# Optimization experiments

Measured on AMD Instinct MI355X. Metric: run time of the kernel, lower is better.

The kernel has to match this reference:

```python
import jax, jax.numpy as jnp
import numpy as np

B, S = 2, 2048
HID = 2560
NH, NKV, HD = 20, 5, 128
GROUPS = NH // NKV  # 4
THETA = 500000.0
RMS_EPS = 1e-6  # RMSNorm default eps used for attn_sub_norm
NEG_INF = -1e9


def pack_ternary(key, M, K):
    """Pack ternary weights {-1,0,1} (stored as trits {0,1,2}) into SIMD
    block-interleaved uint8 layout: per 128-elem block, byte j holds
    weights j+0 (bits 6:7), j+32 (4:5), j+64 (2:3), j+96 (0:1)."""
    t = jax.random.randint(key, (M, K), 0, 3).astype(jnp.uint8)
    t = t.reshape(M, K // 128, 4, 32)
    byte = (t[:, :, 0] << 6) | (t[:, :, 1] << 4) | (t[:, :, 2] << 2) | t[:, :, 3]
    return byte.reshape(M, K // 4)


def unpack_ternary(packed):
    """Inverse of pack_ternary -> float weights in {-1,0,1}. (M, K//4) -> (M, K)."""
    M, Kp = packed.shape
    nb = Kp // 32
    b = packed.reshape(M, nb, 32)
    fields = jnp.stack([(b >> 6) & 3, (b >> 4) & 3, (b >> 2) & 3, b & 3], axis=2)
    return fields.reshape(M, nb * 128).astype(jnp.float32) - 1.0


def bitlinear(x, packed, scale):
    w = unpack_ternary(packed) * scale  # (out, in)
    return jnp.einsum('bsi,oi->bso', x, w)


def rotate_half(x):
    h = x.shape[-1] // 2
    return jnp.concatenate([-x[..., h:], x[..., :h]], axis=-1)


def rms_norm(x, w, eps=RMS_EPS):
    var = jnp.mean(jnp.square(x.astype(jnp.float32)), axis=-1, keepdims=True)
    return (w * (x * jax.lax.rsqrt(var + eps))).astype(x.dtype)


def setup_inputs() -> dict:
    key = jax.random.key(0)
    ks = jax.random.split(key, 6)
    hidden_states = jax.random.normal(ks[0], (B, S, HID), dtype=jnp.float32)
    causal = jnp.tril(jnp.ones((S, S), dtype=bool))
    attention_mask = jnp.where(causal, 0.0, NEG_INF).astype(jnp.float32)[None, None]
    return {
        'hidden_states': hidden_states,
        'attention_mask': attention_mask,
        'q_w': pack_ternary(ks[1], NH * HD, HID),
        'k_w': pack_ternary(ks[2], NKV * HD, HID),
        'v_w': pack_ternary(ks[3], NKV * HD, HID),
        'o_w': pack_ternary(ks[4], HID, NH * HD),
        'q_scale': jnp.float32(0.02),
        'k_scale': jnp.float32(0.02),
        'v_scale': jnp.float32(0.02),
        'o_scale': jnp.float32(0.02),
        'attn_norm_w': jnp.ones((NH * HD,), dtype=jnp.float32),
    }


def reference(hidden_states, attention_mask, q_w, k_w, v_w, o_w,
              q_scale, k_scale, v_scale, o_scale, attn_norm_w):
    bsz, seq_len, _ = hidden_states.shape
    q = bitlinear(hidden_states, q_w, q_scale)
    k = bitlinear(hidden_states, k_w, k_scale)
    v = bitlinear(hidden_states, v_w, v_scale)
    q = q.reshape(bsz, seq_len, NH, HD).transpose(0, 2, 1, 3)    # (b,h,s,d)
    k = k.reshape(bsz, seq_len, NKV, HD).transpose(0, 2, 1, 3)
    v = v.reshape(bsz, seq_len, NKV, HD).transpose(0, 2, 1, 3)
    # rotary embedding
    inv_freq = 1.0 / (THETA ** (jnp.arange(0, HD, 2, dtype=jnp.float32) / HD))
    t = jnp.arange(seq_len, dtype=jnp.float32)
    freqs = t[:, None] * inv_freq[None, :]            # (s, d/2)
    emb = jnp.concatenate([freqs, freqs], axis=-1)    # (s, d)
    cos, sin = jnp.cos(emb), jnp.sin(emb)
    q = q * cos + rotate_half(q) * sin
    k = k * cos + rotate_half(k) * sin
    # GQA: repeat kv heads
    k = jnp.repeat(k, GROUPS, axis=1)
    v = jnp.repeat(v, GROUPS, axis=1)
    scores = jnp.einsum('bhqd,bhkd->bhqk', q, k) / np.sqrt(HD).astype(np.float32)
    scores = scores + attention_mask
    attn = jax.nn.softmax(scores.astype(jnp.float32), axis=-1).astype(q.dtype)
    out = jnp.einsum('bhqk,bhkd->bhqd', attn, v)
    out = out.transpose(0, 2, 1, 3).reshape(bsz, seq_len, NH * HD)
    out = rms_norm(out, attn_norm_w)
    return bitlinear(out, o_w, o_scale)
```

## Files before the change

kernel.cpp:

```cpp
#include <hip/hip_runtime.h>
#include <cstdint>
#include <cstddef>

typedef __bf16 bf16x8 __attribute__((ext_vector_type(8)));
typedef float  f32x4  __attribute__((ext_vector_type(4)));
typedef int    i32x4  __attribute__((ext_vector_type(4)));
typedef unsigned short u16x4 __attribute__((ext_vector_type(4)));

#define DEV __device__ __forceinline__
#define NEGINF (-__builtin_inff())

DEV uint16_t f2bf(float f) {
  union { float f; uint32_t u; } v; v.f = f;
  uint32_t u = v.u;
  u += 0x7FFFu + ((u >> 16) & 1u);
  return (uint16_t)(u >> 16);
}
DEV float bf2f(uint16_t h) {
  union { uint32_t u; float f; } v; v.u = ((uint32_t)h) << 16;
  return v.f;
}

DEV void gload_lds16(const void* g, void* l) {
  __builtin_amdgcn_global_load_lds(
      (const __attribute__((address_space(1))) void*)g,
      (__attribute__((address_space(3))) void*)l, 16, 0, 0);
}


__global__ void k_f32_to_bf16(const float* __restrict__ in, uint16_t* __restrict__ out, int n4) {
  int i = blockIdx.x * blockDim.x + threadIdx.x;
  if (i >= n4) return;
  f32x4 v = *(const f32x4*)(in + (size_t)i * 4);
  u16x4 o;
  o[0] = f2bf(v[0]); o[1] = f2bf(v[1]); o[2] = f2bf(v[2]); o[3] = f2bf(v[3]);
  *(u16x4*)(out + (size_t)i * 4) = o;
}

__global__ void k_unpack(const uint32_t* __restrict__ p, uint16_t* __restrict__ w, int total, int Kq) {
  int idx = blockIdx.x * blockDim.x + threadIdx.x;
  if (idx >= total) return;
  int row = idx / Kq, pc = idx - row * Kq;
  int blk = pc >> 5, j = pc & 31;
  uint32_t b = p[idx] & 0xFFu;
  size_t base = (size_t)row * (size_t)(Kq * 4) + (size_t)blk * 128 + j;
  w[base]      = f2bf((float)((b >> 6) & 3u) - 1.0f);
  w[base + 32] = f2bf((float)((b >> 4) & 3u) - 1.0f);
  w[base + 64] = f2bf((float)((b >> 2) & 3u) - 1.0f);
  w[base + 96] = f2bf((float)(b & 3u) - 1.0f);
}

__global__ void k_rope_table(float* __restrict__ cosT, float* __restrict__ sinT) {
  int idx = blockIdx.x * blockDim.x + threadIdx.x;
  int s = idx >> 6, i = idx & 63;
  float inv = expf((float)i * (-13.122363377404328f / 64.0f));
  float fr = (float)s * inv;
  cosT[idx] = cosf(fr);
  sinT[idx] = sinf(fr);
}

__global__ void k_rope(uint16_t* __restrict__ buf, const float* __restrict__ cosT,
                       const float* __restrict__ sinT, int H, int total) {
  int idx = blockIdx.x * blockDim.x + threadIdx.x;
  if (idx >= total) return;
  int d = idx & 63;
  int t = idx >> 6;
  int h = t % H;
  int row = t / H;
  int s = row & 2047;
  size_t base = (size_t)row * (size_t)(H * 128) + (size_t)h * 128 + d;
  float x1 = bf2f(buf[base]), x2 = bf2f(buf[base + 64]);
  float c = cosT[(s << 6) + d], sn = sinT[(s << 6) + d];
  buf[base]      = f2bf(x1 * c - x2 * sn);
  buf[base + 64] = f2bf(x2 * c + x1 * sn);
}

template<int MODE>
__global__ __launch_bounds__(256, 2)
void k_gemm(const uint16_t* __restrict__ A, const uint16_t* __restrict__ W,
            uint16_t* __restrict__ Qo, uint16_t* __restrict__ Ko, uint16_t* __restrict__ Vo,
            float* __restrict__ Fo,
            const float* __restrict__ s0p, const float* __restrict__ s1p, const float* __restrict__ s2p,
            int M, int N, int K)
{
  __shared__ uint16_t As[128 * 64];
  __shared__ uint16_t Bs[128 * 64];
  const int tid = threadIdx.x;
  const int n0 = blockIdx.x * 128, m0 = blockIdx.y * 128;
  const int lane = tid & 63, w = tid >> 6;
  const int wm = (w >> 1) * 64, wn = (w & 1) * 64;
  const int lr = lane & 15, lg = lane >> 4, lk = lg * 8;
  const size_t K2 = (size_t)K * 2;
  f32x4 acc[4][4] = {};

  const int srow = tid >> 3;
  const int cprime = ((tid & 7) * 16) ^ ((srow & 7) << 4);
  const uint8_t* Ag = (const uint8_t*)A + (size_t)(m0 + srow) * K2 + cprime;
  const uint8_t* Wg = (const uint8_t*)W + (size_t)(n0 + srow) * K2 + cprime;
  char* Al = (char*)As + w * 1024;
  char* Bl = (char*)Bs + w * 1024;

  for (size_t k0b = 0; k0b < K2; k0b += 128) {
    #pragma unroll
    for (int i = 0; i < 4; ++i)
      gload_lds16(Ag + (size_t)(i * 32) * K2 + k0b, Al + i * 4096);
    #pragma unroll
    for (int i = 0; i < 4; ++i)
      gload_lds16(Wg + (size_t)(i * 32) * K2 + k0b, Bl + i * 4096);
    __syncthreads();
    #pragma unroll
    for (int kc = 0; kc < 64; kc += 32) {
      bf16x8 a[4], b[4];
      #pragma unroll
      for (int i = 0; i < 4; ++i) {
        const int r = wm + i * 16 + lr;
        a[i] = *(const bf16x8*)((const char*)As + r * 128 + (((kc + lk) * 2) ^ ((r & 7) << 4)));
      }
      #pragma unroll
      for (int j = 0; j < 4; ++j) {
        const int r = wn + j * 16 + lr;
        b[j] = *(const bf16x8*)((const char*)Bs + r * 128 + (((kc + lk) * 2) ^ ((r & 7) << 4)));
      }
      #pragma unroll
      for (int i = 0; i < 4; ++i)
        #pragma unroll
        for (int j = 0; j < 4; ++j)
          acc[i][j] = __builtin_amdgcn_mfma_f32_16x16x32_bf16(a[i], b[j], acc[i][j], 0, 0, 0);
    }
    __syncthreads();
  }

  if (MODE == 0) {
    const float qs = *s0p, ks = *s1p, vs = *s2p;
    #pragma unroll
    for (int i = 0; i < 4; ++i) {
      const int rowb = m0 + wm + i * 16 + lg * 4;
      #pragma unroll
      for (int j = 0; j < 4; ++j) {
        const int col = n0 + wn + j * 16 + lr;
        #pragma unroll
        for (int r = 0; r < 4; ++r) {
          const int rr = rowb + r;
          const float v = acc[i][j][r];
          if (col < 2560) {
            Qo[(size_t)rr * 2560 + col] = f2bf(v * qs);
          } else if (col < 3200) {
            Ko[(size_t)rr * 640 + (col - 2560)] = f2bf(v * ks);
          } else {
            const int n2 = col - 3200;
            const int kvh = n2 >> 7, d = n2 & 127;
            const int bb = rr >> 11, ss = rr & 2047;
            Vo[(((size_t)(bb * 5 + kvh) * 128 + d) << 11) + ss] = f2bf(v * vs);
          }
        }
      }
    }
  } else {
    const float os = *s0p;
    #pragma unroll
    for (int i = 0; i < 4; ++i) {
      const int rowb = m0 + wm + i * 16 + lg * 4;
      #pragma unroll
      for (int j = 0; j < 4; ++j) {
        const int col = n0 + wn + j * 16 + lr;
        #pragma unroll
        for (int r = 0; r < 4; ++r)
          Fo[(size_t)(rowb + r) * N + col] = acc[i][j][r] * os;
      }
    }
  }
}

__global__ __launch_bounds__(256)
void k_attn(const uint16_t* __restrict__ Q, const uint16_t* __restrict__ Kb,
            const uint16_t* __restrict__ Vt, uint16_t* __restrict__ Ob)
{
  __shared__ char Klds[2][16384];
  __shared__ char Vlds[2][16384];
  __shared__ uint16_t p_lds[4][16][88];

  const int lin = blockIdx.x + (blockIdx.y << 6);
  const int gslot = (lin & 7) * 80 + (lin >> 3);
  const int p = gslot & 63;
  const int bk = gslot >> 6;
  const int b = bk / 5, kvh = bk - b * 5;

  const int tid = threadIdx.x, lane = tid & 63, w = tid >> 6;
  const int lr = lane & 15, lg = lane >> 4, lk = lg * 8;
  const int h = kvh * 4 + w;
  uint16_t (*pl)[88] = p_lds[w];
  const int kswz = (lr & 7) << 4;

  const uint8_t* Kg = (const uint8_t*)(Kb + (size_t)b * 2048 * 640 + (size_t)kvh * 128);
  const uint8_t* Vg = (const uint8_t*)(Vt + ((size_t)(b * 5 + kvh) * 128) * 2048);

  const int krow = tid >> 4;
  const int kcol = ((tid & 15) * 16) ^ ((krow & 7) << 4);
  const int vrow = tid >> 3;
  const int vcol = ((tid & 7) * 16) ^ ((vrow & 7) << 4);
  const int dst16 = tid * 16;

  const float C = 0.127531019577f;

  #pragma unroll 1
  for (int sel = 0; sel < 2; ++sel) {
    const int st = sel ? (127 - p) : p;
    const int q0 = st * 16;
    const int ns = (q0 + 79) >> 6;

    bf16x8 qf[4];
    {
      const size_t qbase = ((size_t)(b * 2048 + q0 + lr)) * 2560 + (size_t)h * 128 + lk;
      #pragma unroll
      for (int c = 0; c < 4; ++c) qf[c] = *(const bf16x8*)&Q[qbase + c * 32];
    }
    asm volatile("s_waitcnt vmcnt(0)" ::: "memory");

    {
      const uint8_t* Ks = Kg + (size_t)krow * 1280 + kcol;
      const uint8_t* Vs = Vg + (size_t)vrow * 4096 + vcol;
      char* Kd = Klds[0] + dst16;
      char* Vd = Vlds[0] + dst16;
      #pragma unroll
      for (int i = 0; i < 4; ++i) gload_lds16(Ks + (size_t)i * 16 * 1280, Kd + i * 4096);
      #pragma unroll
      for (int i = 0; i < 4; ++i) gload_lds16(Vs + (size_t)i * 32 * 4096, Vd + i * 4096);
    }

    int cur = 0;
    float m = NEGINF, l = 0.f;
    f32x4 oa[8] = {};

    #pragma unroll 1
    for (int stp = 0; stp < ns; ++stp) {
      const int k0 = stp * 64;
      if (stp + 1 < ns) {
        const int kn = k0 + 64;
        const uint8_t* Ks = Kg + (size_t)(kn + krow) * 1280 + kcol;
        const uint8_t* Vs = Vg + (size_t)vrow * 4096 + (size_t)kn * 2 + vcol;
        char* Kd = Klds[cur ^ 1] + dst16;
        char* Vd = Vlds[cur ^ 1] + dst16;
        #pragma unroll
        for (int i = 0; i < 4; ++i) gload_lds16(Ks + (size_t)i * 16 * 1280, Kd + i * 4096);
        #pragma unroll
        for (int i = 0; i < 4; ++i) gload_lds16(Vs + (size_t)i * 32 * 4096, Vd + i * 4096);
        asm volatile("s_waitcnt vmcnt(8)" ::: "memory");
      } else {
        asm volatile("s_waitcnt vmcnt(0)" ::: "memory");
      }
      __syncthreads();

      const char* Kc = Klds[cur];
      const char* Vc = Vlds[cur];
      const bool bound = (k0 + 64 >= q0 + 16);

      f32x4 sa[4] = {};
      #pragma unroll
      for (int t = 0; t < 4; ++t) {
        #pragma unroll
        for (int c = 0; c < 4; ++c) {
          bf16x8 kf = *(const bf16x8*)(Kc + (t * 16 + lr) * 256 + ((c * 64 + lg * 16) ^ kswz));
          sa[t] = __builtin_amdgcn_mfma_f32_16x16x32_bf16(kf, qf[c], sa[t], 0, 0, 0);
        }
      }
      float u[16];
      if (bound) {
        #pragma unroll
        for (int t = 0; t < 4; ++t)
          #pragma unroll
          for (int r = 0; r < 4; ++r)
            u[t * 4 + r] = (k0 + t * 16 + lg * 4 + r <= q0 + lr) ? sa[t][r] * C : NEGINF;
      } else {
        #pragma unroll
        for (int t = 0; t < 4; ++t)
          #pragma unroll
          for (int r = 0; r < 4; ++r)
            u[t * 4 + r] = sa[t][r] * C;
      }
      float m01 = fmaxf(u[0], u[1]),   m23 = fmaxf(u[2], u[3]);
      float m45 = fmaxf(u[4], u[5]),   m67 = fmaxf(u[6], u[7]);
      float m89 = fmaxf(u[8], u[9]),   mab = fmaxf(u[10], u[11]);
      float mcd = fmaxf(u[12], u[13]), mef = fmaxf(u[14], u[15]);
      float mx = fmaxf(fmaxf(fmaxf(m01, m23), fmaxf(m45, m67)),
                       fmaxf(fmaxf(m89, mab), fmaxf(mcd, mef)));
      mx = fmaxf(mx, __shfl_xor(mx, 16));
      mx = fmaxf(mx, __shfl_xor(mx, 32));
      const float mn = fmaxf(m, mx);
      const float resc = __builtin_exp2f(m - mn);
      m = mn;
      float pv[16];
      #pragma unroll
      for (int i = 0; i < 16; ++i) pv[i] = __builtin_exp2f(u[i] - mn);
      float s0 = (pv[0] + pv[1]) + (pv[2] + pv[3]);
      float s1 = (pv[4] + pv[5]) + (pv[6] + pv[7]);
      float s2 = (pv[8] + pv[9]) + (pv[10] + pv[11]);
      float s3 = (pv[12] + pv[13]) + (pv[14] + pv[15]);
      l = l * resc + ((s0 + s1) + (s2 + s3));
      #pragma unroll
      for (int t = 0; t < 4; ++t) {
        union { __bf16 b4[4]; unsigned long long u64; } pk;
        #pragma unroll
        for (int r = 0; r < 4; ++r) pk.b4[r] = (__bf16)pv[t * 4 + r];
        *(unsigned long long*)&pl[lr][t * 16 + lg * 4] = pk.u64;
      }
      #pragma unroll
      for (int dc = 0; dc < 8; ++dc) {
        oa[dc][0] *= resc; oa[dc][1] *= resc; oa[dc][2] *= resc; oa[dc][3] *= resc;
      }
      bf16x8 pa0 = *(const bf16x8*)&pl[lr][lk];
      bf16x8 pa1 = *(const bf16x8*)&pl[lr][32 + lk];
      #pragma unroll
      for (int dc = 0; dc < 8; ++dc) {
        bf16x8 vf0 = *(const bf16x8*)(Vc + (dc * 16 + lr) * 128 + ((lg * 16) ^ kswz));
        bf16x8 vf1 = *(const bf16x8*)(Vc + (dc * 16 + lr) * 128 + ((64 + lg * 16) ^ kswz));
        oa[dc] = __builtin_amdgcn_mfma_f32_16x16x32_bf16(vf0, pa0, oa[dc], 0, 0, 0);
        oa[dc] = __builtin_amdgcn_mfma_f32_16x16x32_bf16(vf1, pa1, oa[dc], 0, 0, 0);
      }
      __syncthreads();
      cur ^= 1;
    }

    float lf = l;
    lf += __shfl_xor(lf, 16);
    lf += __shfl_xor(lf, 32);
    const float inv = 1.0f / lf;
    const size_t obase = ((size_t)(b * 2048 + q0 + lr)) * 2560 + (size_t)h * 128;
    #pragma unroll
    for (int dc = 0; dc < 8; ++dc) {
      union { __bf16 b4[4]; unsigned long long u64; } ok;
      #pragma unroll
      for (int r = 0; r < 4; ++r) ok.b4[r] = (__bf16)(oa[dc][r] * inv);
      *(unsigned long long*)&Ob[obase + dc * 16 + lg * 4] = ok.u64;
    }
  }
}

__global__ __launch_bounds__(256)
void k_rmsnorm(const uint16_t* __restrict__ X, const float* __restrict__ g, uint16_t* __restrict__ Y)
{
  const int row = blockIdx.x;
  const int tid = threadIdx.x;
  const uint16_t* x = X + (size_t)row * 2560;
  float ss = 0.f;
  #pragma unroll
  for (int it = 0; it < 10; ++it) {
    const int i = tid + it * 256;
    const float v = bf2f(x[i]);
    ss += v * v;
  }
  #pragma unroll
  for (int off = 1; off < 64; off <<= 1) ss += __shfl_xor(ss, off, 64);
  __shared__ float sred[4];
  if ((tid & 63) == 0) sred[tid >> 6] = ss;
  __syncthreads();
  const float tot = sred[0] + sred[1] + sred[2] + sred[3];
  const float rs = rsqrtf(tot * (1.0f / 2560.0f) + 1e-6f);
  uint16_t* y = Y + (size_t)row * 2560;
  #pragma unroll
  for (int it = 0; it < 10; ++it) {
    const int i = tid + it * 256;
    y[i] = f2bf(bf2f(x[i]) * rs * g[i]);
  }
}

extern "C" void kernel_launch(void* const* d_in, const int* in_sizes, int n_in,
                              void* d_out, int out_size, void* d_ws, size_t ws_size,
                              hipStream_t stream)
{
  const float*    x     = (const float*)d_in[0];
  const uint32_t* qw    = (const uint32_t*)d_in[2];
  const uint32_t* kw    = (const uint32_t*)d_in[3];
  const uint32_t* vw    = (const uint32_t*)d_in[4];
  const uint32_t* ow    = (const uint32_t*)d_in[5];
  const float*    qs    = (const float*)d_in[6];
  const float*    ks    = (const float*)d_in[7];
  const float*    vs    = (const float*)d_in[8];
  const float*    os    = (const float*)d_in[9];
  const float*    gnorm = (const float*)d_in[10];

  char* ws = (char*)d_ws;
  uint16_t* xb   = (uint16_t*)(ws + 0);
  uint16_t* wqkv = (uint16_t*)(ws + 20971520);
  uint16_t* owb  = (uint16_t*)(ws + 40632320);
  float*    cosT = (float*)   (ws + 53739520);
  float*    sinT = (float*)   (ws + 54263808);
  uint16_t* Qb   = (uint16_t*)(ws + 54788096);
  uint16_t* Kb   = (uint16_t*)(ws + 75759616);
  uint16_t* Vt   = (uint16_t*)(ws + 81002496);

  k_f32_to_bf16<<<10240, 256, 0, stream>>>(x, xb, 2621440);
  k_unpack<<<6400, 256, 0, stream>>>(qw, wqkv, 1638400, 640);
  k_unpack<<<1600, 256, 0, stream>>>(kw, wqkv + (size_t)2560 * 2560, 409600, 640);
  k_unpack<<<1600, 256, 0, stream>>>(vw, wqkv + (size_t)3200 * 2560, 409600, 640);
  k_unpack<<<6400, 256, 0, stream>>>(ow, owb, 1638400, 640);
  k_rope_table<<<512, 256, 0, stream>>>(cosT, sinT);

  k_gemm<0><<<dim3(30, 32), 256, 0, stream>>>(xb, wqkv, Qb, Kb, Vt, nullptr,
                                              qs, ks, vs, 4096, 3840, 2560);
  k_rope<<<20480, 256, 0, stream>>>(Qb, cosT, sinT, 20, 5242880);
  k_rope<<<5120, 256, 0, stream>>>(Kb, cosT, sinT, 5, 1310720);

  k_attn<<<dim3(64, 10), 256, 0, stream>>>(Qb, Kb, Vt, xb);

  k_rmsnorm<<<4096, 256, 0, stream>>>(xb, gnorm, Qb);

  k_gemm<1><<<dim3(20, 32), 256, 0, stream>>>(Qb, owb, nullptr, nullptr, nullptr,
                                              (float*)d_out, os, nullptr, nullptr,
                                              4096, 2560, 2560);
}
```

Measured before the change: 335.3 us.

## Double-buffer GEMM LDS tiles and load attention V directly to registers

The GEMM now double-buffers its A/W LDS tiles, prefetching the next K-slab while computing on the current one, with a single barrier per iteration instead of two. In attention, V is no longer staged through LDS. Each wave loads its V fragments straight from global memory into registers, and only K is double-buffered in LDS. The next K prefetch is issued mid-iteration, and s_setprio is raised around the MFMA blocks. This aims to hide global latency and cut LDS traffic and barriers. The cost is more registers and uncoalesced, duplicated V global reads across the four waves.

```diff
diff --git a/kernel.cpp b/kernel.cpp
--- a/kernel.cpp
+++ b/kernel.cpp
@@ -83,8 +83,8 @@
             const float* __restrict__ s0p, const float* __restrict__ s1p, const float* __restrict__ s2p,
             int M, int N, int K)
 {
-  __shared__ uint16_t As[128 * 64];
-  __shared__ uint16_t Bs[128 * 64];
+  __shared__ uint16_t As[2][128 * 64];
+  __shared__ uint16_t Bs[2][128 * 64];
   const int tid = threadIdx.x;
   const int n0 = blockIdx.x * 128, m0 = blockIdx.y * 128;
   const int lane = tid & 63, w = tid >> 6;
@@ -97,29 +97,44 @@
   const int cprime = ((tid & 7) * 16) ^ ((srow & 7) << 4);
   const uint8_t* Ag = (const uint8_t*)A + (size_t)(m0 + srow) * K2 + cprime;
   const uint8_t* Wg = (const uint8_t*)W + (size_t)(n0 + srow) * K2 + cprime;
-  char* Al = (char*)As + w * 1024;
-  char* Bl = (char*)Bs + w * 1024;
-
-  for (size_t k0b = 0; k0b < K2; k0b += 128) {
-    #pragma unroll
-    for (int i = 0; i < 4; ++i)
-      gload_lds16(Ag + (size_t)(i * 32) * K2 + k0b, Al + i * 4096);
-    #pragma unroll
-    for (int i = 0; i < 4; ++i)
-      gload_lds16(Wg + (size_t)(i * 32) * K2 + k0b, Bl + i * 4096);
-    __syncthreads();
+  const int woff = w * 1024;
+
+  #pragma unroll
+  for (int i = 0; i < 4; ++i)
+    gload_lds16(Ag + (size_t)(i * 32) * K2, (char*)As[0] + woff + i * 4096);
+  #pragma unroll
+  for (int i = 0; i < 4; ++i)
+    gload_lds16(Wg + (size_t)(i * 32) * K2, (char*)Bs[0] + woff + i * 4096);
+
+  const int NT = K >> 6;
+  int cur = 0;
+  #pragma unroll 1
+  for (int t = 0; t < NT; ++t) {
+    asm volatile("s_waitcnt vmcnt(0)" ::: "memory");
+    __builtin_amdgcn_s_barrier();
+    if (t + 1 < NT) {
+      const size_t kb = (size_t)(t + 1) * 128;
+      #pragma unroll
+      for (int i = 0; i < 4; ++i)
+        gload_lds16(Ag + (size_t)(i * 32) * K2 + kb, (char*)As[cur ^ 1] + woff + i * 4096);
+      #pragma unroll
+      for (int i = 0; i < 4; ++i)
+        gload_lds16(Wg + (size_t)(i * 32) * K2 + kb, (char*)Bs[cur ^ 1] + woff + i * 4096);
+    }
+    const char* Ac = (const char*)As[cur];
+    const char* Bc = (const char*)Bs[cur];
     #pragma unroll
     for (int kc = 0; kc < 64; kc += 32) {
       bf16x8 a[4], b[4];
       #pragma unroll
       for (int i = 0; i < 4; ++i) {
         const int r = wm + i * 16 + lr;
-        a[i] = *(const bf16x8*)((const char*)As + r * 128 + (((kc + lk) * 2) ^ ((r & 7) << 4)));
+        a[i] = *(const bf16x8*)(Ac + r * 128 + (((kc + lk) * 2) ^ ((r & 7) << 4)));
       }
       #pragma unroll
       for (int j = 0; j < 4; ++j) {
         const int r = wn + j * 16 + lr;
-        b[j] = *(const bf16x8*)((const char*)Bs + r * 128 + (((kc + lk) * 2) ^ ((r & 7) << 4)));
+        b[j] = *(const bf16x8*)(Bc + r * 128 + (((kc + lk) * 2) ^ ((r & 7) << 4)));
       }
       #pragma unroll
       for (int i = 0; i < 4; ++i)
@@ -127,7 +142,7 @@
         for (int j = 0; j < 4; ++j)
           acc[i][j] = __builtin_amdgcn_mfma_f32_16x16x32_bf16(a[i], b[j], acc[i][j], 0, 0, 0);
     }
-    __syncthreads();
+    cur ^= 1;
   }
 
   if (MODE == 0) {
@@ -176,7 +191,6 @@
             const uint16_t* __restrict__ Vt, uint16_t* __restrict__ Ob)
 {
   __shared__ char Klds[2][16384];
-  __shared__ char Vlds[2][16384];
   __shared__ uint16_t p_lds[4][16][88];
 
   const int lin = blockIdx.x + (blockIdx.y << 6);
@@ -191,13 +205,11 @@
   uint16_t (*pl)[88] = p_lds[w];
   const int kswz = (lr & 7) << 4;
 
-  const uint8_t* Kg = (const uint8_t*)(Kb + (size_t)b * 2048 * 640 + (size_t)kvh * 128);
-  const uint8_t* Vg = (const uint8_t*)(Vt + ((size_t)(b * 5 + kvh) * 128) * 2048);
+  const uint8_t*  Kg    = (const uint8_t*)(Kb + (size_t)b * 2048 * 640 + (size_t)kvh * 128);
+  const uint16_t* Vbase = Vt + ((size_t)(b * 5 + kvh) * 128) * 2048;
 
   const int krow = tid >> 4;
   const int kcol = ((tid & 15) * 16) ^ ((krow & 7) << 4);
-  const int vrow = tid >> 3;
-  const int vcol = ((tid & 7) * 16) ^ ((vrow & 7) << 4);
   const int dst16 = tid * 16;
 
   const float C = 0.127531019577f;
@@ -208,23 +220,20 @@
     const int q0 = st * 16;
     const int ns = (q0 + 79) >> 6;
 
+    __builtin_amdgcn_s_barrier();
+
     bf16x8 qf[4];
     {
       const size_t qbase = ((size_t)(b * 2048 + q0 + lr)) * 2560 + (size_t)h * 128 + lk;
       #pragma unroll
       for (int c = 0; c < 4; ++c) qf[c] = *(const bf16x8*)&Q[qbase + c * 32];
     }
-    asm volatile("s_waitcnt vmcnt(0)" ::: "memory");
 
     {
       const uint8_t* Ks = Kg + (size_t)krow * 1280 + kcol;
-      const uint8_t* Vs = Vg + (size_t)vrow * 4096 + vcol;
-      char* Kd = Klds[0] + dst16;
-      char* Vd = Vlds[0] + dst16;
-      #pragma unroll
-      for (int i = 0; i < 4; ++i) gload_lds16(Ks + (size_t)i * 16 * 1280, Kd + i * 4096);
-      #pragma unroll
-      for (int i = 0; i < 4; ++i) gload_lds16(Vs + (size_t)i * 32 * 4096, Vd + i * 4096);
+      #pragma unroll
+      for (int i = 0; i < 4; ++i)
+        gload_lds16(Ks + (size_t)i * 16 * 1280, Klds[0] + dst16 + i * 4096);
     }
 
     int cur = 0;
@@ -234,26 +243,18 @@
     #pragma unroll 1
     for (int stp = 0; stp < ns; ++stp) {
       const int k0 = stp * 64;
-      if (stp + 1 < ns) {
-        const int kn = k0 + 64;
-        const uint8_t* Ks = Kg + (size_t)(kn + krow) * 1280 + kcol;
-        const uint8_t* Vs = Vg + (size_t)vrow * 4096 + (size_t)kn * 2 + vcol;
-        char* Kd = Klds[cur ^ 1] + dst16;
-        char* Vd = Vlds[cur ^ 1] + dst16;
-        #pragma unroll
-        for (int i = 0; i < 4; ++i) gload_lds16(Ks + (size_t)i * 16 * 1280, Kd + i * 4096);
-        #pragma unroll
-        for (int i = 0; i < 4; ++i) gload_lds16(Vs + (size_t)i * 32 * 4096, Vd + i * 4096);
-        asm volatile("s_waitcnt vmcnt(8)" ::: "memory");
-      } else {
-        asm volatile("s_waitcnt vmcnt(0)" ::: "memory");
-      }
-      __syncthreads();
+      asm volatile("s_waitcnt vmcnt(0)" ::: "memory");
+      __builtin_amdgcn_s_barrier();
+
+      bf16x8 v0[8];
+      #pragma unroll
+      for (int dc = 0; dc < 8; ++dc)
+        v0[dc] = *(const bf16x8*)&Vbase[(size_t)(dc * 16 + lr) * 2048 + k0 + lk];
 
       const char* Kc = Klds[cur];
-      const char* Vc = Vlds[cur];
       const bool bound = (k0 + 64 >= q0 + 16);
 
+      __builtin_amdgcn_s_setprio(1);
       f32x4 sa[4] = {};
       #pragma unroll
       for (int t = 0; t < 4; ++t) {
@@ -263,6 +264,8 @@
           sa[t] = __builtin_amdgcn_mfma_f32_16x16x32_bf16(kf, qf[c], sa[t], 0, 0, 0);
         }
       }
+      __builtin_amdgcn_s_setprio(0);
+
       float u[16];
       if (bound) {
         #pragma unroll
@@ -285,6 +288,20 @@
                        fmaxf(fmaxf(m89, mab), fmaxf(mcd, mef)));
       mx = fmaxf(mx, __shfl_xor(mx, 16));
       mx = fmaxf(mx, __shfl_xor(mx, 32));
+
+      bf16x8 v1[8];
+      #pragma unroll
+      for (int dc = 0; dc < 8; ++dc)
+        v1[dc] = *(const bf16x8*)&Vbase[(size_t)(dc * 16 + lr) * 2048 + k0 + 32 + lk];
+      __builtin_amdgcn_sched_barrier(0);
+      if (stp + 1 < ns) {
+        const uint8_t* Ks = Kg + (size_t)(k0 + 64 + krow) * 1280 + kcol;
+        #pragma unroll
+        for (int i = 0; i < 4; ++i)
+          gload_lds16(Ks + (size_t)i * 16 * 1280, Klds[cur ^ 1] + dst16 + i * 4096);
+      }
+      __builtin_amdgcn_sched_barrier(0);
+
       const float mn = fmaxf(m, mx);
       const float resc = __builtin_exp2f(m - mn);
       m = mn;
@@ -309,14 +326,14 @@
       }
       bf16x8 pa0 = *(const bf16x8*)&pl[lr][lk];
       bf16x8 pa1 = *(const bf16x8*)&pl[lr][32 + lk];
-      #pragma unroll
-      for (int dc = 0; dc < 8; ++dc) {
-        bf16x8 vf0 = *(const bf16x8*)(Vc + (dc * 16 + lr) * 128 + ((lg * 16) ^ kswz));
-        bf16x8 vf1 = *(const bf16x8*)(Vc + (dc * 16 + lr) * 128 + ((64 + lg * 16) ^ kswz));
-        oa[dc] = __builtin_amdgcn_mfma_f32_16x16x32_bf16(vf0, pa0, oa[dc], 0, 0, 0);
-        oa[dc] = __builtin_amdgcn_mfma_f32_16x16x32_bf16(vf1, pa1, oa[dc], 0, 0, 0);
-      }
-      __syncthreads();
+      __builtin_amdgcn_s_setprio(1);
+      #pragma unroll
+      for (int dc = 0; dc < 8; ++dc)
+        oa[dc] = __builtin_amdgcn_mfma_f32_16x16x32_bf16(v0[dc], pa0, oa[dc], 0, 0, 0);
+      #pragma unroll
+      for (int dc = 0; dc < 8; ++dc)
+        oa[dc] = __builtin_amdgcn_mfma_f32_16x16x32_bf16(v1[dc], pa1, oa[dc], 0, 0, 0);
+      __builtin_amdgcn_s_setprio(0);
       cur ^= 1;
     }
 
```

Result: slower. 465.8 us (+38.9%).
